# Kernel tuning notes

Hardware: AMD Instinct MI355X
Metric: run time of the kernel (lower is better)

Reference implementation:

```python
import jax, jax.numpy as jnp
import numpy as np

B, T, V, E, H = 16, 32, 1003, 100, 2048


def setup_inputs() -> dict:
    key = jax.random.key(0)
    ks = jax.random.split(key, 16)
    s = 0.02
    n = lambda k, shape: (jax.random.normal(k, shape, jnp.float32) * s)
    tokens = jax.random.randint(ks[0], (B, T), 0, V, dtype=jnp.int32)
    return {
        "tokens": tokens,
        "emb": n(ks[1], (V, E)),
        "W1": n(ks[2], (E, 4 * H)), "U1": n(ks[3], (H, 4 * H)), "b1": jnp.zeros((4 * H,), jnp.float32),
        "W2": n(ks[4], (H, 4 * H)), "U2": n(ks[5], (H, 4 * H)), "b2": jnp.zeros((4 * H,), jnp.float32),
        "W3": n(ks[6], (H, 4 * H)), "U3": n(ks[7], (H, 4 * H)), "b3": jnp.zeros((4 * H,), jnp.float32),
        "Wd1": n(ks[8], (H, H)), "bd1": jnp.zeros((H,), jnp.float32),
        "Wd2": n(ks[9], (H, V)), "bd2": jnp.zeros((V,), jnp.float32),
    }


def masked_lstm(x, mask, W, U, b):
    """Keras-semantics masked LSTM. x: [B,T,D], mask: [B,T] bool.
    Masked steps carry h,c through unchanged (cuDNN-incompatible path).
    Returns (all_h: [B,T,H], last_h: [B,H])."""
    Hd = U.shape[0]
    Bd = x.shape[0]
    # precompute input projections for all timesteps at once: [T,B,4H]
    xz = jnp.einsum('btd,dh->tbh', x, W) + b
    m_t = jnp.swapaxes(mask, 0, 1)  # [T,B]

    def step(carry, inp):
        h, c = carry
        zx, mt = inp
        z = zx + h @ U  # [B,4H]
        i, f, g, o = jnp.split(z, 4, axis=-1)
        i = jax.nn.sigmoid(i)
        f = jax.nn.sigmoid(f)
        g = jnp.tanh(g)
        o = jax.nn.sigmoid(o)
        c_new = f * c + i * g
        h_new = o * jnp.tanh(c_new)
        m = mt[:, None]
        h_new = jnp.where(m, h_new, h)
        c_new = jnp.where(m, c_new, c)
        return (h_new, c_new), h_new

    init = (jnp.zeros((Bd, Hd), x.dtype), jnp.zeros((Bd, Hd), x.dtype))
    (h_last, _), hs = jax.lax.scan(step, init, (xz, m_t))
    return jnp.swapaxes(hs, 0, 1), h_last


def reference(tokens, emb, W1, U1, b1, W2, U2, b2, W3, U3, b3, Wd1, bd1, Wd2, bd2):
    mask = tokens != 0  # mask_zero=True semantics
    x = emb[tokens]  # [B,T,E]
    x, _ = masked_lstm(x, mask, W1, U1, b1)
    x, _ = masked_lstm(x, mask, W2, U2, b2)
    _, h = masked_lstm(x, mask, W3, U3, b3)  # return_sequences=False -> last (carried) state
    y = h @ Wd1 + bd1  # Dense, linear activation
    logits = y @ Wd2 + bd2
    return jax.nn.softmax(logits, axis=-1)
```

## Files before the change

### kernel.cpp

```cpp
#include <hip/hip_runtime.h>
#include <hip/hip_bf16.h>
#include <cstddef>

#define BB 16
#define TT 32
#define VV 1003
#define EE 100
#define HH 2048
#define G4 8192

typedef __attribute__((ext_vector_type(4))) float f32x4;
typedef unsigned char u8;

#define SA 64.0f
#define SB 128.0f
#define DESCALE 1.220703125e-4f

__device__ __forceinline__ unsigned pk_lo(unsigned old, float a, float b) {
  return (unsigned)__builtin_amdgcn_cvt_pk_fp8_f32(a, b, (int)old, false);
}
__device__ __forceinline__ unsigned pk_hi(unsigned old, float a, float b) {
  return (unsigned)__builtin_amdgcn_cvt_pk_fp8_f32(a, b, (int)old, true);
}
__device__ __forceinline__ u8 cvt1fp8(float a) {
  return (u8)(__builtin_amdgcn_cvt_pk_fp8_f32(a, 0.f, 0, false) & 0xff);
}
__device__ __forceinline__ long mklong(unsigned lo, unsigned hi) {
  return (long)(((unsigned long long)hi << 32) | lo);
}

__global__ __launch_bounds__(256) void embed_frag(
    const int* __restrict__ tokens, const float* __restrict__ emb,
    u8* __restrict__ xf) {
  int i = blockIdx.x * 256 + threadIdx.x;
  if (i >= TT * BB * 128) return;
  int e = i & 127, b = (i >> 7) & 15, t = i >> 11;
  float v = 0.f;
  if (e < EE) v = emb[(size_t)tokens[b * TT + t] * EE + e] * SA;
  int kt = e >> 5, kk = e & 31;
  int lane = (kk >> 3) * 16 + b, j = kk & 7;
  xf[(size_t)t * 2048 + (size_t)(kt >> 1) * 1024 + lane * 16 + (kt & 1) * 8 + j] =
      cvt1fp8(v);
}

__device__ __forceinline__ void split_body(
    u8* __restrict__ ldb,
    const float* __restrict__ src, u8* __restrict__ dst,
    int Kreal, int nkt2, int pair, int ct0, int tid) {
  int r0 = pair * 64;
#pragma unroll
  for (int p = 0; p < 4; p++) {
    int c4 = tid & 63, rq = p * 4 + (tid >> 6);
    int c = c4 * 4;
    int g = c >> 6;
    int rel = c & 63;
    int row = rq * 4;
    float4 v[4];
#pragma unroll
    for (int i = 0; i < 4; i++) {
      int r = r0 + row + i;
      v[i] = (r < Kreal)
          ? *(const float4*)&src[(size_t)r * G4 + (size_t)g * HH + ct0 * 4 + rel]
          : make_float4(0.f, 0.f, 0.f, 0.f);
    }
#pragma unroll
    for (int j = 0; j < 4; j++) {
      unsigned w = 0;
      w = pk_lo(w, ((const float*)&v[0])[j] * SB, ((const float*)&v[1])[j] * SB);
      w = pk_hi(w, ((const float*)&v[2])[j] * SB, ((const float*)&v[3])[j] * SB);
      int cc = c + j;
      *(unsigned*)&ldb[cc * 72 + g * 8 + row] = w;
    }
  }
  __syncthreads();
  int L = tid & 63;
  int cl = L & 15, gg = cl >> 2, hq = cl & 3;
  int row0 = (L >> 4) * 8;
#pragma unroll
  for (int pass = 0; pass < 4; pass++) {
    int ctr = (tid >> 6) + pass * 4;
    int cc = gg * 64 + ctr * 4 + hq;
    const u8* bp = &ldb[cc * 72 + gg * 8];
    uint2 h0 = *(const uint2*)&bp[row0];
    uint2 h1 = *(const uint2*)&bp[32 + row0];
    *(uint4*)&dst[((size_t)(ct0 + ctr) * nkt2 + pair) * 1024 + L * 16] =
        make_uint4(h0.x, h0.y, h1.x, h1.y);
  }
}

__device__ __forceinline__ void split_body_512(
    u8* __restrict__ ldb,
    const float* __restrict__ src, u8* __restrict__ dst,
    int nkt2, int pair, int ct0, int tid) {
  int r0 = pair * 64;
  int c4 = tid & 63;
  int c = c4 * 4;
  int g = c >> 6;
  int rel = c & 63;
  int rg = tid >> 6;
  const float* colbase = src + (size_t)g * HH + ct0 * 4 + rel;
  float4 v[8];
#pragma unroll
  for (int i = 0; i < 8; i++)
    v[i] = *(const float4*)&colbase[(size_t)(r0 + rg * 8 + i) * G4];
#pragma unroll
  for (int j = 0; j < 4; j++) {
    unsigned w0 = 0, w1 = 0;
    w0 = pk_lo(w0, ((const float*)&v[0])[j] * SB, ((const float*)&v[1])[j] * SB);
    w0 = pk_hi(w0, ((const float*)&v[2])[j] * SB, ((const float*)&v[3])[j] * SB);
    w1 = pk_lo(w1, ((const float*)&v[4])[j] * SB, ((const float*)&v[5])[j] * SB);
    w1 = pk_hi(w1, ((const float*)&v[6])[j] * SB, ((const float*)&v[7])[j] * SB);
    int cc = c + j;
    *(unsigned*)&ldb[cc * 72 + g * 8 + rg * 8] = w0;
    *(unsigned*)&ldb[cc * 72 + g * 8 + rg * 8 + 4] = w1;
  }
  __syncthreads();
  int L = tid & 63;
  int cl = L & 15, gg = cl >> 2, hq = cl & 3;
  int row0 = (L >> 4) * 8;
#pragma unroll
  for (int pass = 0; pass < 2; pass++) {
    int ctr = (tid >> 6) + pass * 8;
    int cc = gg * 64 + ctr * 4 + hq;
    const u8* bp = &ldb[cc * 72 + gg * 8];
    uint2 h0 = *(const uint2*)&bp[row0];
    uint2 h1 = *(const uint2*)&bp[32 + row0];
    *(uint4*)&dst[((size_t)(ct0 + ctr) * nkt2 + pair) * 1024 + L * 16] =
        make_uint4(h0.x, h0.y, h1.x, h1.y);
  }
}

__global__ __launch_bounds__(256) void split_wu(
    const float* __restrict__ srcW, u8* __restrict__ dstW, int KrealW, int nkt2W,
    const float* __restrict__ srcU, u8* __restrict__ dstU) {
  __shared__ __align__(16) u8 ldb[256 * 72 + 16];
  int tid = threadIdx.x;
  int bx = blockIdx.x, ct0 = blockIdx.y * 16;
  if (bx < nkt2W)
    split_body(ldb, srcW, dstW, KrealW, nkt2W, bx, ct0, tid);
  else
    split_body(ldb, srcU, dstU, HH, 32, bx - nkt2W, ct0, tid);
}

__global__ __launch_bounds__(512) void gemm_mfma(
    const u8* __restrict__ af, int t_stride, int nkt2,
    const u8* __restrict__ wfrag, const float* __restrict__ bias,
    float* __restrict__ xz,
    unsigned* __restrict__ hzero,
    unsigned* __restrict__ hcz) {
  __shared__ __align__(16) u8 Bs[3][8][1024];
  int tid = threadIdx.x;
  int w = tid >> 6, L = tid & 63;
  int ct0 = blockIdx.x * 8;
  int t_a = blockIdx.y * 4 + (w & 3);
  int nt0 = (w >> 2) * 4;

  if (blockIdx.y == 0) {
    if (tid < 128) hzero[blockIdx.x * 128 + tid] = 0u;
    hcz[blockIdx.x * 1024 + tid] = 0u;
    hcz[blockIdx.x * 1024 + 512 + tid] = 0u;
  }

  f32x4 acc[4];
#pragma unroll
  for (int i = 0; i < 4; i++) acc[i] = (f32x4){0.f, 0.f, 0.f, 0.f};
  const u8* Ah = af + (size_t)t_a * t_stride + L * 16;

  int s_nt = tid >> 6, boff = (tid & 63) * 16;

  {
    uint4 t0 = *(const uint4*)&wfrag[((size_t)(ct0 + s_nt) * nkt2 + 0) * 1024 + boff];
    *(uint4*)&Bs[0][s_nt][boff] = t0;
    if (nkt2 > 1) {
      uint4 t1 = *(const uint4*)&wfrag[((size_t)(ct0 + s_nt) * nkt2 + 1) * 1024 + boff];
      *(uint4*)&Bs[1][s_nt][boff] = t1;
    }
  }
  __syncthreads();

  for (int s = 0; s < nkt2; s++) {
    uint4 nx;
    bool pf = (s + 2 < nkt2);
    if (pf)
      nx = *(const uint4*)&wfrag[((size_t)(ct0 + s_nt) * nkt2 + s + 2) * 1024 + boff];
    int buf = s % 3;
    uint4 a = *(const uint4*)(Ah + (size_t)s * 1024);
    long a0 = mklong(a.x, a.y), a1 = mklong(a.z, a.w);
#pragma unroll
    for (int i = 0; i < 4; i++) {
      uint4 bb = *(const uint4*)&Bs[buf][nt0 + i][L * 16];
      acc[i] = __builtin_amdgcn_mfma_f32_16x16x32_fp8_fp8(a0, mklong(bb.x, bb.y), acc[i], 0, 0, 0);
      acc[i] = __builtin_amdgcn_mfma_f32_16x16x32_fp8_fp8(a1, mklong(bb.z, bb.w), acc[i], 0, 0, 0);
    }
    if (pf) *(uint4*)&Bs[(s + 2) % 3][s_nt][boff] = nx;
    __syncthreads();
  }

  int nq = L >> 4, hl = L & 15;
#pragma unroll
  for (int i = 0; i < 4; i++) {
    int ctg = ct0 + nt0 + i;
    int gcol = (hl >> 2) * HH + ctg * 4 + (hl & 3);
    float bv = bias[gcol];
#pragma unroll
    for (int r = 0; r < 4; r++) {
      int b = nq * 4 + r;
      xz[((size_t)t_a * 16 + b) * G4 + ctg * 16 + hl] = acc[i][r] * DESCALE + bv;
    }
  }
}

__global__ __launch_bounds__(512, 8) void lstm_step(
    const u8* __restrict__ Ufrag,
    const float* __restrict__ xzt,
    const u8* __restrict__ hf_in,
    u8* __restrict__ hf_out,
    const float* __restrict__ hT_in,
    float* __restrict__ hT_out,
    float* __restrict__ c,
    const int* __restrict__ tokens, int t,
    const float* __restrict__ srcW, u8* __restrict__ dstW,
    const float* __restrict__ srcU, u8* __restrict__ dstU) {
  __shared__ __align__(16) u8 smem[18960];
  int tid = threadIdx.x;

  if (blockIdx.x >= 512) {
    int ext = blockIdx.x - 512;
    int unit = 2 * t + (ext >> 5);
    int ct0 = (ext & 31) * 16;
    if (unit < 32)
      split_body_512(smem, srcW, dstW, 32, unit, ct0, tid);
    else
      split_body_512(smem, srcU, dstU, 32, unit - 32, ct0, tid);
    return;
  }

  float (*red)[16][16] = (float (*)[16][16])smem;
  float (*zs)[16] = (float (*)[16])(smem + 8192);
  int w = tid >> 6, L = tid & 63;
  int ct = blockIdx.x;

  float xzv = 0.f;
  if (tid < 256) xzv = xzt[(size_t)(tid >> 4) * G4 + ct * 16 + (tid & 15)];
  float c_old = 0.f, h_old = 0.f;
  int tok = 1;
  if (tid < 64) {
    int b = tid >> 2, hq = tid & 3;
    int hu = ct * 4 + hq;
    c_old = c[(size_t)b * HH + hu];
    h_old = hT_in[(size_t)hu * BB + b];
    tok = tokens[b * TT + t];
  }

  f32x4 acc = {0.f, 0.f, 0.f, 0.f};
  const u8* Ub = Ufrag + ((size_t)ct * 32 + w * 4) * 1024 + L * 16;
  const u8* Hb = hf_in + (size_t)(w * 4) * 1024 + L * 16;

#pragma unroll
  for (int i = 0; i < 4; i++) {
    uint4 u = *(const uint4*)(Ub + i * 1024);
    uint4 h = *(const uint4*)(Hb + i * 1024);
    acc = __builtin_amdgcn_mfma_f32_16x16x32_fp8_fp8(mklong(h.x, h.y), mklong(u.x, u.y), acc, 0, 0, 0);
    acc = __builtin_amdgcn_mfma_f32_16x16x32_fp8_fp8(mklong(h.z, h.w), mklong(u.z, u.w), acc, 0, 0, 0);
  }
#pragma unroll
  for (int r = 0; r < 4; r++) red[w][(L >> 4) * 4 + r][L & 15] = acc[r];
  __syncthreads();

  if (tid < 256) {
    int b = tid >> 4, cl = tid & 15;
    float s = 0.f;
#pragma unroll
    for (int q = 0; q < 8; q++) s += red[q][b][cl];
    zs[b][cl] = s * DESCALE + xzv;
  }
  __syncthreads();

  if (tid < 64) {
    int b = tid >> 2, hq = tid & 3;
    int hu = ct * 4 + hq;
    float z0 = zs[b][0 + hq];
    float z1 = zs[b][4 + hq];
    float z2 = zs[b][8 + hq];
    float z3 = zs[b][12 + hq];
    float ig = 1.f / (1.f + expf(-z0));
    float fg = 1.f / (1.f + expf(-z1));
    float gt = tanhf(z2);
    float og = 1.f / (1.f + expf(-z3));
    float cn = fg * c_old + ig * gt;
    float hn = og * tanhf(cn);
    if (tok == 0) {
      cn = c_old;
      hn = h_old;
    }
    c[(size_t)b * HH + hu] = cn;
    hT_out[(size_t)hu * BB + b] = hn;
    int kt2 = hu >> 5, kk = hu & 31;
    int lane2 = (kk >> 3) * 16 + b, jj = kk & 7;
    hf_out[(size_t)(kt2 >> 1) * 1024 + lane2 * 16 + (kt2 & 1) * 8 + jj] =
        cvt1fp8(hn * SA);
  }
}

__global__ __launch_bounds__(256) void head_partial(
    const float* __restrict__ XT, const float* __restrict__ W,
    float* __restrict__ partial, int N) {
  __shared__ float xs[2048];
  int tid = threadIdx.x;
  int k0 = blockIdx.y * 128;
  const float* src = XT + (size_t)k0 * 16;
  for (int i = tid; i < 2048; i += 256) xs[i] = src[i];
  __syncthreads();
  int kg = tid >> 6, lane = tid & 63;
  int col = blockIdx.x * 64 + lane;
  if (col >= N) return;
  float acc[16];
#pragma unroll
  for (int b = 0; b < 16; b++) acc[b] = 0.f;
  const float* Wp = W + (size_t)(k0 + kg * 32) * N + col;
  const float* xp = xs + kg * 32 * 16;
  for (int kk = 0; kk < 32; kk++) {
    float wv = Wp[(size_t)kk * N];
#pragma unroll
    for (int b = 0; b < 16; b++) acc[b] = fmaf(xp[kk * 16 + b], wv, acc[b]);
  }
  int chunk = blockIdx.y * 4 + kg;
#pragma unroll
  for (int b = 0; b < 16; b++)
    partial[((size_t)chunk * 16 + b) * N + col] = acc[b];
}

__global__ __launch_bounds__(256) void head_reduce(
    const float* __restrict__ partial, const float* __restrict__ bias,
    float* __restrict__ out, int N, int sc, int sb) {
  int i = blockIdx.x * 256 + threadIdx.x;
  if (i >= 16 * N) return;
  int b = i / N, col = i - b * N;
  float s = bias[col];
#pragma unroll 8
  for (int ch = 0; ch < 64; ch++) s += partial[((size_t)ch * 16 + b) * N + col];
  out[(size_t)col * sc + (size_t)b * sb] = s;
}

__global__ __launch_bounds__(256) void softmax_rows(
    const float* __restrict__ logits, float* __restrict__ out, int N) {
  __shared__ float buf[1024];
  __shared__ float wred[4];
  __shared__ float rmax, rsum;
  int b = blockIdx.x, tid = threadIdx.x;
  float m = -1e30f;
  for (int v = tid; v < N; v += 256) {
    float x = logits[(size_t)b * N + v];
    buf[v] = x;
    m = fmaxf(m, x);
  }
  for (int o = 32; o > 0; o >>= 1) m = fmaxf(m, __shfl_down(m, o, 64));
  if ((tid & 63) == 0) wred[tid >> 6] = m;
  __syncthreads();
  if (tid == 0) rmax = fmaxf(fmaxf(wred[0], wred[1]), fmaxf(wred[2], wred[3]));
  __syncthreads();
  float s = 0.f;
  for (int v = tid; v < N; v += 256) {
    float e = expf(buf[v] - rmax);
    buf[v] = e;
    s += e;
  }
  for (int o = 32; o > 0; o >>= 1) s += __shfl_down(s, o, 64);
  if ((tid & 63) == 0) wred[tid >> 6] = s;
  __syncthreads();
  if (tid == 0) rsum = wred[0] + wred[1] + wred[2] + wred[3];
  __syncthreads();
  float inv = 1.f / rsum;
  for (int v = tid; v < N; v += 256) out[(size_t)b * N + v] = buf[v] * inv;
}

extern "C" void kernel_launch(void* const* d_in, const int* in_sizes, int n_in,
                              void* d_out, int out_size, void* d_ws, size_t ws_size,
                              hipStream_t stream) {
  const int*   tokens = (const int*)d_in[0];
  const float* emb  = (const float*)d_in[1];
  const float* W1   = (const float*)d_in[2];
  const float* U1   = (const float*)d_in[3];
  const float* b1   = (const float*)d_in[4];
  const float* W2   = (const float*)d_in[5];
  const float* U2   = (const float*)d_in[6];
  const float* b2   = (const float*)d_in[7];
  const float* W3   = (const float*)d_in[8];
  const float* U3   = (const float*)d_in[9];
  const float* b3   = (const float*)d_in[10];
  const float* Wd1  = (const float*)d_in[11];
  const float* bd1  = (const float*)d_in[12];
  const float* Wd2  = (const float*)d_in[13];
  const float* bd2  = (const float*)d_in[14];
  float* out = (float*)d_out;

  char* base = (char*)d_ws;
  size_t off = 0;
  auto carve = [&](size_t bytes) -> char* {
    char* p = base + off;
    off += (bytes + 255) & ~(size_t)255;
    return p;
  };
  float* xz      = (float*)carve((size_t)TT * BB * G4 * 4);
  u8*    allhf0  = (u8*)carve(33ull * 32768);
  u8*    allhf1  = (u8*)carve(33ull * 32768);
  u8*    allhf2  = (u8*)carve(33ull * 32768);
  u8*    xfrag   = (u8*)carve((size_t)TT * 2048);
  u8*    wf0     = (u8*)carve(512ull * 64 * 512);
  u8*    uf0     = (u8*)carve(512ull * 64 * 512);
  u8*    wf1     = (u8*)carve(512ull * 64 * 512);
  u8*    uf1     = (u8*)carve(512ull * 64 * 512);
  float* hT0     = (float*)carve(2 * HH * BB * 4);
  float* cbuf    = hT0 + HH * BB;
  float* hT1     = (float*)carve(HH * BB * 4);
  float* yT      = (float*)carve(HH * BB * 4);
  float* logits  = (float*)carve(BB * 1024 * 4);
  float* partial = (float*)carve(64ull * 16 * HH * 4);

  u8* allhf[3] = {allhf0, allhf1, allhf2};
  const float* Us[3] = {U1, U2, U3};
  const float* Ws[3] = {W1, W2, W3};
  const float* bs[3] = {b1, b2, b3};
  float* hping[2] = {hT0, hT1};
  u8* wfl[3] = {wf0, wf1, wf0};
  u8* ufl[3] = {uf0, uf1, uf0};

  embed_frag<<<dim3(256), 256, 0, stream>>>(tokens, emb, xfrag);

  split_wu<<<dim3(2 + 32, 32), 256, 0, stream>>>(Ws[0], wf0, EE, 2, Us[0], uf0);

  for (int layer = 0; layer < 3; layer++) {
    const u8* af;
    int t_stride, nkt2W;
    if (layer == 0) {
      af = xfrag; t_stride = 2048; nkt2W = 2;
    } else {
      af = allhf[layer - 1] + 32768;
      t_stride = 32768; nkt2W = 32;
    }
    gemm_mfma<<<dim3(64, 8), 512, 0, stream>>>(
        af, t_stride, nkt2W, wfl[layer], bs[layer], xz,
        (unsigned*)allhf[layer], (unsigned*)hT0);

    bool hide = (layer < 2);
    int grid = hide ? 576 : 512;
    const float* sW = hide ? Ws[layer + 1] : Ws[layer];
    u8* dW = wfl[layer + 1 == 3 ? 0 : layer + 1];
    const float* sU = hide ? Us[layer + 1] : Us[layer];
    u8* dU = ufl[layer + 1 == 3 ? 0 : layer + 1];
    for (int t = 0; t < TT; t++) {
      lstm_step<<<dim3(grid), 512, 0, stream>>>(
          ufl[layer], xz + (size_t)t * BB * G4,
          allhf[layer] + (size_t)t * 32768, allhf[layer] + (size_t)(t + 1) * 32768,
          hping[t & 1], hping[(t + 1) & 1], cbuf, tokens, t,
          sW, dW, sU, dU);
    }
  }

  head_partial<<<dim3(HH / 64, 16), 256, 0, stream>>>(hT0, Wd1, partial, HH);
  head_reduce<<<dim3((16 * HH + 255) / 256), 256, 0, stream>>>(partial, bd1, yT, HH, 16, 1);
  head_partial<<<dim3((VV + 63) / 64, 16), 256, 0, stream>>>(yT, Wd2, partial, VV);
  head_reduce<<<dim3((16 * VV + 255) / 256), 256, 0, stream>>>(partial, bd2, logits, VV, 1, VV);
  softmax_rows<<<dim3(BB), 256, 0, stream>>>(logits, out, VV);
}
```

Before: 603.1 us.

## Move next-layer weight conversion into the GEMM launch and widen LSTM step blocks

The fp8 fragment conversion of the next layer's W and U moves out of the per-timestep LSTM launches and into extra blocks of the input-projection GEMM launch. Previously that work was spread over 32 step kernels. The recurrent step kernel now uses 1024 threads (16 waves), each doing half as many MFMAs, with a 16-way shared-memory reduction. This aims to shorten the latency-bound serial step kernels, at the cost of a larger GEMM launch and a larger reduction.

Result: faster. 580.0 us (-3.8%).

```diff
diff --git a/kernel.cpp b/kernel.cpp
--- a/kernel.cpp
+++ b/kernel.cpp
@@ -142,23 +142,40 @@
     split_body(ldb, srcU, dstU, HH, 32, bx - nkt2W, ct0, tid);
 }
 
-__global__ __launch_bounds__(512) void gemm_mfma(
+__global__ __launch_bounds__(512) void gemm_split(
     const u8* __restrict__ af, int t_stride, int nkt2,
     const u8* __restrict__ wfrag, const float* __restrict__ bias,
     float* __restrict__ xz,
     unsigned* __restrict__ hzero,
-    unsigned* __restrict__ hcz) {
-  __shared__ __align__(16) u8 Bs[3][8][1024];
+    unsigned* __restrict__ hcz,
+    const float* __restrict__ srcWn, u8* __restrict__ dstWn,
+    const float* __restrict__ srcUn, u8* __restrict__ dstUn) {
+  __shared__ __align__(16) u8 smem[24576];
   int tid = threadIdx.x;
+  int bid = blockIdx.x;
+
+  if (bid >= 512) {
+    int ext = bid - 512;
+    int rem = ext & 1023;
+    int pair = rem & 31, ct0 = (rem >> 5) * 16;
+    if (ext < 1024)
+      split_body_512(smem, srcWn, dstWn, 32, pair, ct0, tid);
+    else
+      split_body_512(smem, srcUn, dstUn, 32, pair, ct0, tid);
+    return;
+  }
+
+  u8 (*Bs)[8][1024] = (u8 (*)[8][1024])smem;
   int w = tid >> 6, L = tid & 63;
-  int ct0 = blockIdx.x * 8;
-  int t_a = blockIdx.y * 4 + (w & 3);
+  int bx = bid & 63, by = bid >> 6;
+  int ct0 = bx * 8;
+  int t_a = by * 4 + (w & 3);
   int nt0 = (w >> 2) * 4;
 
-  if (blockIdx.y == 0) {
-    if (tid < 128) hzero[blockIdx.x * 128 + tid] = 0u;
-    hcz[blockIdx.x * 1024 + tid] = 0u;
-    hcz[blockIdx.x * 1024 + 512 + tid] = 0u;
+  if (by == 0) {
+    if (tid < 128) hzero[bx * 128 + tid] = 0u;
+    hcz[bx * 1024 + tid] = 0u;
+    hcz[bx * 1024 + 512 + tid] = 0u;
   }
 
   f32x4 acc[4];
@@ -210,7 +227,7 @@
   }
 }
 
-__global__ __launch_bounds__(512, 8) void lstm_step(
+__global__ __launch_bounds__(1024, 8) void lstm_step(
     const u8* __restrict__ Ufrag,
     const float* __restrict__ xzt,
     const u8* __restrict__ hf_in,
@@ -218,26 +235,10 @@
     const float* __restrict__ hT_in,
     float* __restrict__ hT_out,
     float* __restrict__ c,
-    const int* __restrict__ tokens, int t,
-    const float* __restrict__ srcW, u8* __restrict__ dstW,
-    const float* __restrict__ srcU, u8* __restrict__ dstU) {
-  __shared__ __align__(16) u8 smem[18960];
-  int tid = threadIdx.x;
-
-  if (blockIdx.x >= 512) {
-    int ext = blockIdx.x - 512;
-    int unit = 2 * t + (ext >> 5);
-    int ct0 = (ext & 31) * 16;
-    if (unit < 32)
-      split_body_512(smem, srcW, dstW, 32, unit, ct0, tid);
-    else
-      split_body_512(smem, srcU, dstU, 32, unit - 32, ct0, tid);
-    return;
-  }
-
-  float (*red)[16][16] = (float (*)[16][16])smem;
-  float (*zs)[16] = (float (*)[16])(smem + 8192);
-  int w = tid >> 6, L = tid & 63;
+    const int* __restrict__ tokens, int t) {
+  __shared__ float red[16][16][16];
+  __shared__ float zs[16][16];
+  int tid = threadIdx.x, w = tid >> 6, L = tid & 63;
   int ct = blockIdx.x;
 
   float xzv = 0.f;
@@ -253,11 +254,11 @@
   }
 
   f32x4 acc = {0.f, 0.f, 0.f, 0.f};
-  const u8* Ub = Ufrag + ((size_t)ct * 32 + w * 4) * 1024 + L * 16;
-  const u8* Hb = hf_in + (size_t)(w * 4) * 1024 + L * 16;
-
-#pragma unroll
-  for (int i = 0; i < 4; i++) {
+  const u8* Ub = Ufrag + ((size_t)ct * 32 + w * 2) * 1024 + L * 16;
+  const u8* Hb = hf_in + (size_t)(w * 2) * 1024 + L * 16;
+
+#pragma unroll
+  for (int i = 0; i < 2; i++) {
     uint4 u = *(const uint4*)(Ub + i * 1024);
     uint4 h = *(const uint4*)(Hb + i * 1024);
     acc = __builtin_amdgcn_mfma_f32_16x16x32_fp8_fp8(mklong(h.x, h.y), mklong(u.x, u.y), acc, 0, 0, 0);
@@ -271,7 +272,7 @@
     int b = tid >> 4, cl = tid & 15;
     float s = 0.f;
 #pragma unroll
-    for (int q = 0; q < 8; q++) s += red[q][b][cl];
+    for (int q = 0; q < 16; q++) s += red[q][b][cl];
     zs[b][cl] = s * DESCALE + xzv;
   }
   __syncthreads();
@@ -406,10 +407,10 @@
   u8*    allhf1  = (u8*)carve(33ull * 32768);
   u8*    allhf2  = (u8*)carve(33ull * 32768);
   u8*    xfrag   = (u8*)carve((size_t)TT * 2048);
-  u8*    wf0     = (u8*)carve(512ull * 64 * 512);
-  u8*    uf0     = (u8*)carve(512ull * 64 * 512);
-  u8*    wf1     = (u8*)carve(512ull * 64 * 512);
-  u8*    uf1     = (u8*)carve(512ull * 64 * 512);
+  u8*    wfA     = (u8*)carve(512ull * 64 * 512);
+  u8*    ufA     = (u8*)carve(512ull * 64 * 512);
+  u8*    wfB     = (u8*)carve(512ull * 64 * 512);
+  u8*    ufB     = (u8*)carve(512ull * 64 * 512);
   float* hT0     = (float*)carve(2 * HH * BB * 4);
   float* cbuf    = hT0 + HH * BB;
   float* hT1     = (float*)carve(HH * BB * 4);
@@ -418,16 +419,15 @@
   float* partial = (float*)carve(64ull * 16 * HH * 4);
 
   u8* allhf[3] = {allhf0, allhf1, allhf2};
-  const float* Us[3] = {U1, U2, U3};
-  const float* Ws[3] = {W1, W2, W3};
   const float* bs[3] = {b1, b2, b3};
   float* hping[2] = {hT0, hT1};
-  u8* wfl[3] = {wf0, wf1, wf0};
-  u8* ufl[3] = {uf0, uf1, uf0};
+  u8* wfl[3] = {wfA, wfB, wfA};
+  u8* ufl[3] = {ufA, ufB, ufA};
+  const float* Wnext[3] = {W2, W3, nullptr};
+  const float* Unext[3] = {U2, U3, nullptr};
 
   embed_frag<<<dim3(256), 256, 0, stream>>>(tokens, emb, xfrag);
-
-  split_wu<<<dim3(2 + 32, 32), 256, 0, stream>>>(Ws[0], wf0, EE, 2, Us[0], uf0);
+  split_wu<<<dim3(2 + 32, 32), 256, 0, stream>>>(W1, wfA, EE, 2, U1, ufA);
 
   for (int layer = 0; layer < 3; layer++) {
     const u8* af;
@@ -438,22 +438,17 @@
       af = allhf[layer - 1] + 32768;
       t_stride = 32768; nkt2W = 32;
     }
-    gemm_mfma<<<dim3(64, 8), 512, 0, stream>>>(
+    int grid = (layer < 2) ? 2560 : 512;
+    gemm_split<<<dim3(grid), 512, 0, stream>>>(
         af, t_stride, nkt2W, wfl[layer], bs[layer], xz,
-        (unsigned*)allhf[layer], (unsigned*)hT0);
-
-    bool hide = (layer < 2);
-    int grid = hide ? 576 : 512;
-    const float* sW = hide ? Ws[layer + 1] : Ws[layer];
-    u8* dW = wfl[layer + 1 == 3 ? 0 : layer + 1];
-    const float* sU = hide ? Us[layer + 1] : Us[layer];
-    u8* dU = ufl[layer + 1 == 3 ? 0 : layer + 1];
+        (unsigned*)allhf[layer], (unsigned*)hT0,
+        Wnext[layer], wfl[layer + 1 < 3 ? layer + 1 : 0],
+        Unext[layer], ufl[layer + 1 < 3 ? layer + 1 : 0]);
     for (int t = 0; t < TT; t++) {
-      lstm_step<<<dim3(grid), 512, 0, stream>>>(
+      lstm_step<<<dim3(512), 1024, 0, stream>>>(
           ufl[layer], xz + (size_t)t * BB * G4,
           allhf[layer] + (size_t)t * 32768, allhf[layer] + (size_t)(t + 1) * 32768,
-          hping[t & 1], hping[(t + 1) & 1], cbuf, tokens, t,
-          sW, dW, sU, dU);
+          hping[t & 1], hping[(t + 1) & 1], cbuf, tokens, t);
     }
   }
 
```
